# Optimization experiments

Measured on AMD Instinct MI355X. Metric: run time of the kernel, lower is better.

The kernel has to match this reference:

```python
import jax, jax.numpy as jnp
import numpy as np

N_NODES = 50000
IN_C, HID_C, OUT_C = 128, 128, 64
N_EDGES = 800000
N_LABEL = 200000
BN_EPS = 1e-5


def setup_inputs() -> dict:
    key = jax.random.key(0)
    ks = jax.random.split(key, 12)
    s = lambda fan_in: 1.0 / np.sqrt(fan_in)
    return {
        "x": jax.random.normal(ks[0], (N_NODES, IN_C), dtype=jnp.float32),
        "edge_index": jax.random.randint(ks[1], (2, N_EDGES), 0, N_NODES, dtype=jnp.int64),
        "edge_label_index": jax.random.randint(ks[2], (2, N_LABEL), 0, N_NODES, dtype=jnp.int64),
        # SAGEConv1: lin_l (neighbor branch, with bias) and lin_r (root branch, no bias)
        "W1l": jax.random.uniform(ks[3], (IN_C, HID_C), jnp.float32, -s(IN_C), s(IN_C)),
        "W1r": jax.random.uniform(ks[4], (IN_C, HID_C), jnp.float32, -s(IN_C), s(IN_C)),
        "b1": jax.random.uniform(ks[5], (HID_C,), jnp.float32, -s(IN_C), s(IN_C)),
        # BatchNorm1d(hidden)
        "gamma": jnp.ones((HID_C,), jnp.float32),
        "beta": jnp.zeros((HID_C,), jnp.float32),
        # SAGEConv2
        "W2l": jax.random.uniform(ks[6], (HID_C, OUT_C), jnp.float32, -s(HID_C), s(HID_C)),
        "W2r": jax.random.uniform(ks[7], (HID_C, OUT_C), jnp.float32, -s(HID_C), s(HID_C)),
        "b2": jax.random.uniform(ks[8], (OUT_C,), jnp.float32, -s(HID_C), s(HID_C)),
    }


def _sage_conv(x, edge_index, Wl, Wr, b):
    # PyG SAGEConv(aggr='mean'): out = lin_l(mean_{j->i} x_j) + lin_r(x_i)
    src, dst = edge_index[0], edge_index[1]
    n = x.shape[0]
    agg = jax.ops.segment_sum(x[src], dst, num_segments=n)          # [N, C]
    cnt = jax.ops.segment_sum(jnp.ones((src.shape[0],), x.dtype), dst, num_segments=n)
    mean = agg / jnp.maximum(cnt, 1.0)[:, None]                     # isolated nodes -> 0
    return mean @ Wl + x @ Wr + b


def _batchnorm(h, gamma, beta):
    mu = jnp.mean(h, axis=0)
    var = jnp.mean((h - mu) ** 2, axis=0)  # biased variance (torch BN training math)
    return gamma * (h - mu) * jax.lax.rsqrt(var + BN_EPS) + beta


def reference(x, edge_index, edge_label_index, W1l, W1r, b1, gamma, beta, W2l, W2r, b2):
    h = _sage_conv(x, edge_index, W1l, W1r, b1)
    h = jax.nn.relu(_batchnorm(h, gamma, beta))
    # dropout is identity in inference mode
    z = _sage_conv(h, edge_index, W2l, W2r, b2)
    src = z[edge_label_index[0]]
    dst = z[edge_label_index[1]]
    return jnp.sum(src * dst, axis=-1)  # [E_label]
```

## Files before the change

kernel.cpp:

```cpp
#include <hip/hip_runtime.h>

constexpr int N_NODES = 50000;
constexpr int IN_C    = 128;
constexpr int HID_C   = 128;
constexpr int OUT_C   = 64;
constexpr int N_EDGES = 800000;
constexpr int N_LABEL = 200000;
constexpr float BN_EPS = 1e-5f;
constexpr int NCHUNK  = (N_NODES + 256) / 256 + 1;
constexpr int BN_BLOCKS = 512;
constexpr int BN_RPH    = 13;

typedef __attribute__((ext_vector_type(8))) short bf16x8;
typedef __attribute__((ext_vector_type(4))) float f32x4;

__device__ __forceinline__ float bf_lo(unsigned v) {
    union { unsigned u; float f; } t; t.u = v << 16; return t.f;
}
__device__ __forceinline__ float bf_hi(unsigned v) {
    union { unsigned u; float f; } t; t.u = v & 0xffff0000u; return t.f;
}
__device__ __forceinline__ float bf1(unsigned short u) {
    union { unsigned u; float f; } t; t.u = ((unsigned)u) << 16; return t.f;
}
__device__ __forceinline__ unsigned short f2bf(float f) {
    union { float f; unsigned u; } t; t.f = f;
    unsigned r = t.u + 0x7fffu + ((t.u >> 16) & 1u);
    return (unsigned short)(r >> 16);
}

__global__ void hist_kernel(const int* __restrict__ dst, int* __restrict__ deg,
                            int* __restrict__ rank) {
    int e = blockIdx.x * blockDim.x + threadIdx.x;
    if (e < N_EDGES) rank[e] = atomicAdd(&deg[dst[e]], 1);
}

__global__ void chunk_sum_kernel(const int* __restrict__ deg, int* __restrict__ bsum) {
    int i = blockIdx.x * 256 + threadIdx.x;
    int v = deg[i];
    #pragma unroll
    for (int o = 32; o > 0; o >>= 1) v += __shfl_down(v, o, 64);
    __shared__ int ws[4];
    if ((threadIdx.x & 63) == 0) ws[threadIdx.x >> 6] = v;
    __syncthreads();
    if (threadIdx.x == 0) bsum[blockIdx.x] = ws[0] + ws[1] + ws[2] + ws[3];
}

__global__ void scan_bsum_kernel(const int* __restrict__ bsum, int* __restrict__ boff) {
    __shared__ int t[256];
    int tid = threadIdx.x;
    t[tid] = (tid < NCHUNK) ? bsum[tid] : 0;
    __syncthreads();
    for (int o = 1; o < 256; o <<= 1) {
        int v = t[tid];
        int add = (tid >= o) ? t[tid - o] : 0;
        __syncthreads();
        t[tid] = v + add;
        __syncthreads();
    }
    boff[tid] = (tid == 0) ? 0 : t[tid - 1];
}

__global__ void scan_final_kernel(const int* __restrict__ deg, const int* __restrict__ boff,
                                  int* __restrict__ off) {
    __shared__ int t[256];
    int tid = threadIdx.x;
    int i = blockIdx.x * 256 + tid;
    int d = deg[i];
    t[tid] = d;
    __syncthreads();
    for (int o = 1; o < 256; o <<= 1) {
        int v = t[tid];
        int add = (tid >= o) ? t[tid - o] : 0;
        __syncthreads();
        t[tid] = v + add;
        __syncthreads();
    }
    int excl = boff[blockIdx.x] + t[tid] - d;
    if (i <= N_NODES) off[i] = excl;
}

__global__ void scatter_kernel(const int* __restrict__ src, const int* __restrict__ dst,
                               const int* __restrict__ off, const int* __restrict__ rank,
                               int* __restrict__ csr_src) {
    int e = blockIdx.x * blockDim.x + threadIdx.x;
    if (e < N_EDGES) csr_src[off[dst[e]] + rank[e]] = src[e];
}

__global__ void prep_B(const float* __restrict__ Wl, const float* __restrict__ Wr,
                       short* __restrict__ Bp, int C) {
    int f = blockIdx.x * 256 + threadIdx.x;
    if (f >= 128 * C) return;
    int HALF = C >> 1;
    int j = f & 7;
    int l = (f >> 3) & 63;
    int ktnt = f >> 9;
    int kt = ktnt & 3, nt = ktnt >> 2;
    int n = nt * 16 + (l & 15);
    int k = kt * 32 + ((l >> 4) << 3) + j;
    float v = (n < HALF) ? Wl[k * HALF + n] : Wr[k * HALF + (n - HALF)];
    Bp[f] = (short)f2bf(v);
}

template <int MODE>
__global__ __launch_bounds__(256) void mfma_gemm(
    const float* __restrict__ A, const short* __restrict__ Bp,
    const float* __restrict__ bias, const float* __restrict__ ss,
    unsigned short* __restrict__ outL,
    float* __restrict__ outHf, unsigned short* __restrict__ outHb)
{
    constexpr int C    = (MODE == 0) ? 256 : 128;
    constexpr int NT   = C / 16;
    constexpr int HALF = C / 2;
    constexpr int CHUNKS = 128 * C / 8;

    __shared__ short sB[128 * C];

    {
        const float4* bp4 = reinterpret_cast<const float4*>(Bp);
        float4* sb4 = reinterpret_cast<float4*>(sB);
        #pragma unroll
        for (int i = 0; i < CHUNKS / 256; ++i)
            sb4[i * 256 + threadIdx.x] = bp4[i * 256 + threadIdx.x];
    }

    int tid  = threadIdx.x;
    int wid  = tid >> 6, lane = tid & 63;
    int m0   = blockIdx.x * 64 + wid * 16;
    int row  = m0 + (lane & 15);
    int rowc = (row < N_NODES) ? row : (N_NODES - 1);
    const float* ap = A + (long long)rowc * 128;
    int kbase = (lane >> 4) * 8;

    bf16x8 a[4];
    #pragma unroll
    for (int kt = 0; kt < 4; ++kt) {
        int k0 = kt * 32 + kbase;
        float4 u0 = *reinterpret_cast<const float4*>(ap + k0);
        float4 u1 = *reinterpret_cast<const float4*>(ap + k0 + 4);
        float v[8] = {u0.x, u0.y, u0.z, u0.w, u1.x, u1.y, u1.z, u1.w};
        if (MODE == 1) {
            float4 s0 = *reinterpret_cast<const float4*>(ss + k0);
            float4 s1 = *reinterpret_cast<const float4*>(ss + k0 + 4);
            float4 t0 = *reinterpret_cast<const float4*>(ss + 128 + k0);
            float4 t1 = *reinterpret_cast<const float4*>(ss + 128 + k0 + 4);
            float sc[8] = {s0.x, s0.y, s0.z, s0.w, s1.x, s1.y, s1.z, s1.w};
            float sh[8] = {t0.x, t0.y, t0.z, t0.w, t1.x, t1.y, t1.z, t1.w};
            #pragma unroll
            for (int j = 0; j < 8; ++j) v[j] = fmaxf(v[j] * sc[j] + sh[j], 0.f);
        }
        #pragma unroll
        for (int j = 0; j < 8; ++j) a[kt][j] = (short)f2bf(v[j]);
    }

    __syncthreads();

    f32x4 acc[NT] = {};
    #pragma unroll
    for (int kt = 0; kt < 4; ++kt) {
        #pragma unroll
        for (int nt = 0; nt < NT; ++nt) {
            bf16x8 b = *reinterpret_cast<const bf16x8*>(
                sB + ((((nt << 2) + kt) * 64 + lane) << 3));
            acc[nt] = __builtin_amdgcn_mfma_f32_16x16x32_bf16(a[kt], b, acc[nt], 0, 0, 0);
        }
    }

    int r0 = m0 + ((lane >> 4) << 2);
    int nl = lane & 15;
    #pragma unroll
    for (int nt = 0; nt < NT; ++nt) {
        int col = nt * 16 + nl;
        float bb = (col >= HALF) ? bias[col - HALF] : 0.f;
        #pragma unroll
        for (int j = 0; j < 4; ++j) {
            int r = r0 + j;
            if (r >= N_NODES) continue;
            float vv = acc[nt][j];
            if (MODE == 0) {
                if (col < HALF) outL[(long long)r * 128 + col] = f2bf(vv);
                else            outHf[(long long)r * 128 + (col - HALF)] = vv + bb;
            } else {
                if (col < HALF) outL[(long long)r * 64 + col] = f2bf(vv);
                else            outHb[(long long)r * 64 + (col - HALF)] = f2bf(vv + bb);
            }
        }
    }
}

__global__ __launch_bounds__(256) void agg_mean_add_128(
    const int* __restrict__ off, const int* __restrict__ csr_src,
    const uint2* __restrict__ y2, float* __restrict__ h) {
    int node = blockIdx.x * 4 + (threadIdx.x >> 6);
    if (node >= N_NODES) return;
    int lane = threadIdx.x & 63;
    int half = lane >> 5;
    int c8   = lane & 31;
    int beg = off[node], end = off[node + 1];
    float s0 = 0.f, s1 = 0.f, s2 = 0.f, s3 = 0.f;
    int i = beg + half;
    for (; i + 6 < end; i += 8) {
        uint2 v0 = y2[(long long)csr_src[i]     * 32 + c8];
        uint2 v1 = y2[(long long)csr_src[i + 2] * 32 + c8];
        uint2 v2 = y2[(long long)csr_src[i + 4] * 32 + c8];
        uint2 v3 = y2[(long long)csr_src[i + 6] * 32 + c8];
        s0 += bf_lo(v0.x) + bf_lo(v1.x) + bf_lo(v2.x) + bf_lo(v3.x);
        s1 += bf_hi(v0.x) + bf_hi(v1.x) + bf_hi(v2.x) + bf_hi(v3.x);
        s2 += bf_lo(v0.y) + bf_lo(v1.y) + bf_lo(v2.y) + bf_lo(v3.y);
        s3 += bf_hi(v0.y) + bf_hi(v1.y) + bf_hi(v2.y) + bf_hi(v3.y);
    }
    for (; i < end; i += 2) {
        uint2 v0 = y2[(long long)csr_src[i] * 32 + c8];
        s0 += bf_lo(v0.x); s1 += bf_hi(v0.x);
        s2 += bf_lo(v0.y); s3 += bf_hi(v0.y);
    }
    s0 += __shfl_down(s0, 32);
    s1 += __shfl_down(s1, 32);
    s2 += __shfl_down(s2, 32);
    s3 += __shfl_down(s3, 32);
    if (half == 0) {
        float inv = (end > beg) ? 1.0f / (float)(end - beg) : 0.f;
        float4* hp = reinterpret_cast<float4*>(h + (long long)node * 128 + c8 * 4);
        float4 hv = *hp;
        hv.x += s0 * inv; hv.y += s1 * inv; hv.z += s2 * inv; hv.w += s3 * inv;
        *hp = hv;
    }
}

__global__ __launch_bounds__(256) void bn_stats_partial(
    const float* __restrict__ h, float* __restrict__ partial) {
    int tid = threadIdx.x;
    int wid = tid >> 6;
    int lane = tid & 63;
    int half = lane >> 5;
    int c4   = lane & 31;
    int hw   = (blockIdx.x << 3) + (wid << 1) + half;
    int r0   = hw * BN_RPH;

    float4 v[BN_RPH];
    #pragma unroll
    for (int j = 0; j < BN_RPH; ++j) {
        int r = r0 + j;
        if (r < N_NODES)
            v[j] = *reinterpret_cast<const float4*>(h + (long long)r * 128 + c4 * 4);
        else
            v[j] = float4{0.f, 0.f, 0.f, 0.f};
    }
    float s[4] = {0.f, 0.f, 0.f, 0.f}, q[4] = {0.f, 0.f, 0.f, 0.f};
    #pragma unroll
    for (int j = 0; j < BN_RPH; ++j) {
        s[0] += v[j].x; q[0] += v[j].x * v[j].x;
        s[1] += v[j].y; q[1] += v[j].y * v[j].y;
        s[2] += v[j].z; q[2] += v[j].z * v[j].z;
        s[3] += v[j].w; q[3] += v[j].w * v[j].w;
    }
    #pragma unroll
    for (int j = 0; j < 4; ++j) {
        s[j] += __shfl_down(s[j], 32);
        q[j] += __shfl_down(q[j], 32);
    }
    __shared__ float ls[4][32][8];
    if (half == 0) {
        #pragma unroll
        for (int j = 0; j < 4; ++j) { ls[wid][c4][j] = s[j]; ls[wid][c4][4 + j] = q[j]; }
    }
    __syncthreads();
    if (tid < 32) {
        #pragma unroll
        for (int j = 0; j < 8; ++j) {
            float a = ls[0][tid][j] + ls[1][tid][j] + ls[2][tid][j] + ls[3][tid][j];
            partial[blockIdx.x * 256 + (j < 4 ? 0 : 128) + tid * 4 + (j & 3)] = a;
        }
    }
}

__global__ void bn_stats_reduce(const float* __restrict__ partial,
                                float* __restrict__ sums) {
    int t = threadIdx.x;
    int b0 = blockIdx.x * (BN_BLOCKS / 16);
    float a = 0.f;
    #pragma unroll 8
    for (int b = b0; b < b0 + BN_BLOCKS / 16; ++b)
        a += partial[b * 256 + t];
    atomicAdd(&sums[t], a);
}

__global__ void bn_finalize_kernel(const float* __restrict__ sums,
                                   const float* __restrict__ gamma,
                                   const float* __restrict__ beta,
                                   float* __restrict__ ss) {
    int c = threadIdx.x;
    float mu  = sums[c] * (1.0f / N_NODES);
    float var = sums[128 + c] * (1.0f / N_NODES) - mu * mu;
    float sc = gamma[c] * rsqrtf(var + BN_EPS);
    ss[c] = sc;
    ss[128 + c] = beta[c] - mu * sc;
}

__global__ __launch_bounds__(256) void agg_mean_add_64(
    const int* __restrict__ off, const int* __restrict__ csr_src,
    const uint2* __restrict__ t2l2, const uint2* __restrict__ t2r2,
    uint2* __restrict__ z2) {
    int node = blockIdx.x * 4 + (threadIdx.x >> 6);
    if (node >= N_NODES) return;
    int lane = threadIdx.x & 63;
    int grp  = lane >> 4;
    int c8   = lane & 15;
    int beg = off[node], end = off[node + 1];
    float s0 = 0.f, s1 = 0.f, s2 = 0.f, s3 = 0.f;
    int i = beg + grp;
    for (; i + 4 < end; i += 8) {
        uint2 v0 = t2l2[(long long)csr_src[i]     * 16 + c8];
        uint2 v1 = t2l2[(long long)csr_src[i + 4] * 16 + c8];
        s0 += bf_lo(v0.x) + bf_lo(v1.x);
        s1 += bf_hi(v0.x) + bf_hi(v1.x);
        s2 += bf_lo(v0.y) + bf_lo(v1.y);
        s3 += bf_hi(v0.y) + bf_hi(v1.y);
    }
    for (; i < end; i += 4) {
        uint2 v0 = t2l2[(long long)csr_src[i] * 16 + c8];
        s0 += bf_lo(v0.x); s1 += bf_hi(v0.x);
        s2 += bf_lo(v0.y); s3 += bf_hi(v0.y);
    }
    s0 += __shfl_down(s0, 16); s1 += __shfl_down(s1, 16);
    s2 += __shfl_down(s2, 16); s3 += __shfl_down(s3, 16);
    s0 += __shfl_down(s0, 32); s1 += __shfl_down(s1, 32);
    s2 += __shfl_down(s2, 32); s3 += __shfl_down(s3, 32);
    if (grp == 0) {
        float inv = (end > beg) ? 1.0f / (float)(end - beg) : 0.f;
        uint2 rv = t2r2[(long long)node * 16 + c8];
        float r0 = bf_lo(rv.x) + s0 * inv;
        float r1 = bf_hi(rv.x) + s1 * inv;
        float r2 = bf_lo(rv.y) + s2 * inv;
        float r3 = bf_hi(rv.y) + s3 * inv;
        uint2 o;
        o.x = (unsigned)f2bf(r0) | ((unsigned)f2bf(r1) << 16);
        o.y = (unsigned)f2bf(r2) | ((unsigned)f2bf(r3) << 16);
        z2[(long long)node * 16 + c8] = o;
    }
}

__global__ void edge_dot_kernel(const int* __restrict__ eli,
                                const unsigned short* __restrict__ z,
                                float* __restrict__ out) {
    long long gid = (long long)blockIdx.x * blockDim.x + threadIdx.x;
    int l = (int)(gid >> 4);
    int lane = (int)(gid & 15);
    if (l >= N_LABEL) return;
    int s = eli[l];
    int d = eli[N_LABEL + l];
    uint2 av = *reinterpret_cast<const uint2*>(z + (long long)s * 64 + lane * 4);
    uint2 bv = *reinterpret_cast<const uint2*>(z + (long long)d * 64 + lane * 4);
    float p = bf_lo(av.x) * bf_lo(bv.x) + bf_hi(av.x) * bf_hi(bv.x)
            + bf_lo(av.y) * bf_lo(bv.y) + bf_hi(av.y) * bf_hi(bv.y);
    p += __shfl_down(p, 8, 16);
    p += __shfl_down(p, 4, 16);
    p += __shfl_down(p, 2, 16);
    p += __shfl_down(p, 1, 16);
    if (lane == 0) out[l] = p;
}

extern "C" void kernel_launch(void* const* d_in, const int* in_sizes, int n_in,
                              void* d_out, int out_size, void* d_ws, size_t ws_size,
                              hipStream_t stream) {
    const float* x     = (const float*)d_in[0];
    const int*   ei    = (const int*)d_in[1];
    const int*   eli   = (const int*)d_in[2];
    const float* W1l   = (const float*)d_in[3];
    const float* W1r   = (const float*)d_in[4];
    const float* b1    = (const float*)d_in[5];
    const float* gamma = (const float*)d_in[6];
    const float* beta  = (const float*)d_in[7];
    const float* W2l   = (const float*)d_in[8];
    const float* W2r   = (const float*)d_in[9];
    const float* b2    = (const float*)d_in[10];
    float* out = (float*)d_out;

    const int* src  = ei;
    const int* dstv = ei + N_EDGES;

    int* ideg  = (int*)d_ws;
    int* ioff  = ideg + 50432;
    int* ibsum = ioff + 50056;
    int* iboff = ibsum + 256;
    int* icsr  = iboff + 256;
    unsigned short* y1  = (unsigned short*)(icsr + 800000);
    float*          h   = (float*)(y1 + 6400000);
    unsigned short* t2l = (unsigned short*)(h + 6400000);
    unsigned short* t2r = t2l + 3200000;
    unsigned short* z   = t2r + 3200000;
    float* sums = (float*)(z + 3200000);
    float* ss   = sums + 256;
    short* Bp1  = (short*)(ss + 256);
    short* Bp2  = Bp1 + 32768;
    float* bnpart = (float*)(Bp2 + 16384);
    int* irank = (int*)y1;

    hipMemsetAsync(ideg, 0, 50432 * sizeof(int), stream);
    hipMemsetAsync(sums, 0, 256 * sizeof(float), stream);

    prep_B<<<(128 * 256 + 255) / 256, 256, 0, stream>>>(W1l, W1r, Bp1, 256);
    prep_B<<<(128 * 128 + 255) / 256, 256, 0, stream>>>(W2l, W2r, Bp2, 128);

    hist_kernel<<<(N_EDGES + 255) / 256, 256, 0, stream>>>(dstv, ideg, irank);
    chunk_sum_kernel<<<NCHUNK, 256, 0, stream>>>(ideg, ibsum);
    scan_bsum_kernel<<<1, 256, 0, stream>>>(ibsum, iboff);
    scan_final_kernel<<<NCHUNK, 256, 0, stream>>>(ideg, iboff, ioff);
    scatter_kernel<<<(N_EDGES + 255) / 256, 256, 0, stream>>>(src, dstv, ioff, irank, icsr);

    const int GEMM_GRID = (N_NODES + 63) / 64;

    mfma_gemm<0><<<GEMM_GRID, 256, 0, stream>>>(x, Bp1, b1, ss, y1, h, nullptr);
    agg_mean_add_128<<<(N_NODES + 3) / 4, 256, 0, stream>>>(
        ioff, icsr, (const uint2*)y1, h);

    bn_stats_partial<<<BN_BLOCKS, 256, 0, stream>>>(h, bnpart);
    bn_stats_reduce<<<16, 256, 0, stream>>>(bnpart, sums);
    bn_finalize_kernel<<<1, 128, 0, stream>>>(sums, gamma, beta, ss);

    mfma_gemm<1><<<GEMM_GRID, 256, 0, stream>>>(h, Bp2, b2, ss, t2l, nullptr, t2r);
    agg_mean_add_64<<<(N_NODES + 3) / 4, 256, 0, stream>>>(
        ioff, icsr, (const uint2*)t2l, (const uint2*)t2r, (uint2*)z);

    edge_dot_kernel<<<((long long)N_LABEL * 16 + 255) / 256, 256, 0, stream>>>(eli, z, out);
}
```

Baseline: 200.7 us.

## Store layer-1 neighbor projection in fp8 and hidden activations in bf16

The layer-1 neighbor-branch GEMM output is now stored as a custom 8-bit float (scaled e4m3-like encoding) instead of bf16, which halves the bytes gathered per edge in the first aggregation. The root-branch hidden tensor h becomes bf16 instead of fp32, so the aggregation read-modify-write, the BN stats pass and the second GEMM's A load all move half the data. The aggregation loop is restructured so four 16-lane groups each read 8 channels per edge. The cost is reduced numerical precision in the intermediate activations, which may push error toward tolerance limits.

```diff
diff --git a/kernel.cpp b/kernel.cpp
--- a/kernel.cpp
+++ b/kernel.cpp
@@ -20,13 +20,25 @@
 __device__ __forceinline__ float bf_hi(unsigned v) {
     union { unsigned u; float f; } t; t.u = v & 0xffff0000u; return t.f;
 }
-__device__ __forceinline__ float bf1(unsigned short u) {
-    union { unsigned u; float f; } t; t.u = ((unsigned)u) << 16; return t.f;
-}
 __device__ __forceinline__ unsigned short f2bf(float f) {
     union { float f; unsigned u; } t; t.f = f;
     unsigned r = t.u + 0x7fffu + ((t.u >> 16) & 1u);
     return (unsigned short)(r >> 16);
+}
+__device__ __forceinline__ unsigned pack2bf(float a, float b) {
+    return (unsigned)f2bf(a) | ((unsigned)f2bf(b) << 16);
+}
+
+__device__ __forceinline__ float fp8_f32(unsigned b) {
+    union { unsigned u; float f; } t;
+    t.u = ((b & 0x80u) << 24) | ((b & 0x7Fu) << 20);
+    return t.f * 0x1p120f;
+}
+__device__ __forceinline__ unsigned f32_fp8(float x) {
+    union { float f; unsigned u; } t; t.f = x * 0x1p-120f;
+    unsigned au = t.u & 0x7FFFFFFFu;
+    unsigned r = au + 0x7FFFFu + ((au >> 20) & 1u);
+    return ((r >> 20) & 0x7Fu) | ((t.u >> 24) & 0x80u);
 }
 
 __global__ void hist_kernel(const int* __restrict__ dst, int* __restrict__ deg,
@@ -104,10 +116,11 @@
 
 template <int MODE>
 __global__ __launch_bounds__(256) void mfma_gemm(
-    const float* __restrict__ A, const short* __restrict__ Bp,
+    const void* __restrict__ Ain, const short* __restrict__ Bp,
     const float* __restrict__ bias, const float* __restrict__ ss,
-    unsigned short* __restrict__ outL,
-    float* __restrict__ outHf, unsigned short* __restrict__ outHb)
+    unsigned char* __restrict__ outFp8,
+    unsigned short* __restrict__ outL16,
+    unsigned short* __restrict__ outH16)
 {
     constexpr int C    = (MODE == 0) ? 256 : 128;
     constexpr int NT   = C / 16;
@@ -129,17 +142,24 @@
     int m0   = blockIdx.x * 64 + wid * 16;
     int row  = m0 + (lane & 15);
     int rowc = (row < N_NODES) ? row : (N_NODES - 1);
-    const float* ap = A + (long long)rowc * 128;
     int kbase = (lane >> 4) * 8;
 
     bf16x8 a[4];
     #pragma unroll
     for (int kt = 0; kt < 4; ++kt) {
         int k0 = kt * 32 + kbase;
-        float4 u0 = *reinterpret_cast<const float4*>(ap + k0);
-        float4 u1 = *reinterpret_cast<const float4*>(ap + k0 + 4);
-        float v[8] = {u0.x, u0.y, u0.z, u0.w, u1.x, u1.y, u1.z, u1.w};
-        if (MODE == 1) {
+        float v[8];
+        if (MODE == 0) {
+            const float* ap = (const float*)Ain + (long long)rowc * 128;
+            float4 u0 = *reinterpret_cast<const float4*>(ap + k0);
+            float4 u1 = *reinterpret_cast<const float4*>(ap + k0 + 4);
+            v[0]=u0.x; v[1]=u0.y; v[2]=u0.z; v[3]=u0.w;
+            v[4]=u1.x; v[5]=u1.y; v[6]=u1.z; v[7]=u1.w;
+        } else {
+            const unsigned short* ap = (const unsigned short*)Ain + (long long)rowc * 128;
+            uint4 w = *reinterpret_cast<const uint4*>(ap + k0);
+            v[0]=bf_lo(w.x); v[1]=bf_hi(w.x); v[2]=bf_lo(w.y); v[3]=bf_hi(w.y);
+            v[4]=bf_lo(w.z); v[5]=bf_hi(w.z); v[6]=bf_lo(w.w); v[7]=bf_hi(w.w);
             float4 s0 = *reinterpret_cast<const float4*>(ss + k0);
             float4 s1 = *reinterpret_cast<const float4*>(ss + k0 + 4);
             float4 t0 = *reinterpret_cast<const float4*>(ss + 128 + k0);
@@ -178,11 +198,11 @@
             if (r >= N_NODES) continue;
             float vv = acc[nt][j];
             if (MODE == 0) {
-                if (col < HALF) outL[(long long)r * 128 + col] = f2bf(vv);
-                else            outHf[(long long)r * 128 + (col - HALF)] = vv + bb;
+                if (col < HALF) outFp8[(long long)r * 128 + col] = (unsigned char)f32_fp8(vv);
+                else            outH16[(long long)r * 128 + (col - HALF)] = f2bf(vv + bb);
             } else {
-                if (col < HALF) outL[(long long)r * 64 + col] = f2bf(vv);
-                else            outHb[(long long)r * 64 + (col - HALF)] = f2bf(vv + bb);
+                if (col < HALF) outL16[(long long)r * 64 + col] = f2bf(vv);
+                else            outH16[(long long)r * 64 + (col - HALF)] = f2bf(vv + bb);
             }
         }
     }
@@ -190,45 +210,50 @@
 
 __global__ __launch_bounds__(256) void agg_mean_add_128(
     const int* __restrict__ off, const int* __restrict__ csr_src,
-    const uint2* __restrict__ y2, float* __restrict__ h) {
+    const uint2* __restrict__ y8, uint4* __restrict__ h4) {
     int node = blockIdx.x * 4 + (threadIdx.x >> 6);
     if (node >= N_NODES) return;
     int lane = threadIdx.x & 63;
-    int half = lane >> 5;
-    int c8   = lane & 31;
+    int grp  = lane >> 4;
+    int c8   = lane & 15;
     int beg = off[node], end = off[node + 1];
-    float s0 = 0.f, s1 = 0.f, s2 = 0.f, s3 = 0.f;
-    int i = beg + half;
-    for (; i + 6 < end; i += 8) {
-        uint2 v0 = y2[(long long)csr_src[i]     * 32 + c8];
-        uint2 v1 = y2[(long long)csr_src[i + 2] * 32 + c8];
-        uint2 v2 = y2[(long long)csr_src[i + 4] * 32 + c8];
-        uint2 v3 = y2[(long long)csr_src[i + 6] * 32 + c8];
-        s0 += bf_lo(v0.x) + bf_lo(v1.x) + bf_lo(v2.x) + bf_lo(v3.x);
-        s1 += bf_hi(v0.x) + bf_hi(v1.x) + bf_hi(v2.x) + bf_hi(v3.x);
-        s2 += bf_lo(v0.y) + bf_lo(v1.y) + bf_lo(v2.y) + bf_lo(v3.y);
-        s3 += bf_hi(v0.y) + bf_hi(v1.y) + bf_hi(v2.y) + bf_hi(v3.y);
-    }
-    for (; i < end; i += 2) {
-        uint2 v0 = y2[(long long)csr_src[i] * 32 + c8];
-        s0 += bf_lo(v0.x); s1 += bf_hi(v0.x);
-        s2 += bf_lo(v0.y); s3 += bf_hi(v0.y);
-    }
-    s0 += __shfl_down(s0, 32);
-    s1 += __shfl_down(s1, 32);
-    s2 += __shfl_down(s2, 32);
-    s3 += __shfl_down(s3, 32);
-    if (half == 0) {
+    float s[8] = {0.f, 0.f, 0.f, 0.f, 0.f, 0.f, 0.f, 0.f};
+    int i = beg + grp;
+    for (; i + 4 < end; i += 8) {
+        uint2 v0 = y8[(long long)csr_src[i]     * 16 + c8];
+        uint2 v1 = y8[(long long)csr_src[i + 4] * 16 + c8];
+        #pragma unroll
+        for (int j = 0; j < 4; ++j) {
+            s[j]     += fp8_f32((v0.x >> (8 * j)) & 0xFFu) + fp8_f32((v1.x >> (8 * j)) & 0xFFu);
+            s[4 + j] += fp8_f32((v0.y >> (8 * j)) & 0xFFu) + fp8_f32((v1.y >> (8 * j)) & 0xFFu);
+        }
+    }
+    for (; i < end; i += 4) {
+        uint2 v0 = y8[(long long)csr_src[i] * 16 + c8];
+        #pragma unroll
+        for (int j = 0; j < 4; ++j) {
+            s[j]     += fp8_f32((v0.x >> (8 * j)) & 0xFFu);
+            s[4 + j] += fp8_f32((v0.y >> (8 * j)) & 0xFFu);
+        }
+    }
+    #pragma unroll
+    for (int j = 0; j < 8; ++j) {
+        s[j] += __shfl_down(s[j], 16);
+        s[j] += __shfl_down(s[j], 32);
+    }
+    if (grp == 0) {
         float inv = (end > beg) ? 1.0f / (float)(end - beg) : 0.f;
-        float4* hp = reinterpret_cast<float4*>(h + (long long)node * 128 + c8 * 4);
-        float4 hv = *hp;
-        hv.x += s0 * inv; hv.y += s1 * inv; hv.z += s2 * inv; hv.w += s3 * inv;
-        *hp = hv;
+        uint4 hv = h4[(long long)node * 16 + c8];
+        hv.x = pack2bf(bf_lo(hv.x) + s[0] * inv, bf_hi(hv.x) + s[1] * inv);
+        hv.y = pack2bf(bf_lo(hv.y) + s[2] * inv, bf_hi(hv.y) + s[3] * inv);
+        hv.z = pack2bf(bf_lo(hv.z) + s[4] * inv, bf_hi(hv.z) + s[5] * inv);
+        hv.w = pack2bf(bf_lo(hv.w) + s[6] * inv, bf_hi(hv.w) + s[7] * inv);
+        h4[(long long)node * 16 + c8] = hv;
     }
 }
 
 __global__ __launch_bounds__(256) void bn_stats_partial(
-    const float* __restrict__ h, float* __restrict__ partial) {
+    const uint2* __restrict__ h2, float* __restrict__ partial) {
     int tid = threadIdx.x;
     int wid = tid >> 6;
     int lane = tid & 63;
@@ -237,22 +262,21 @@
     int hw   = (blockIdx.x << 3) + (wid << 1) + half;
     int r0   = hw * BN_RPH;
 
-    float4 v[BN_RPH];
+    uint2 v[BN_RPH];
     #pragma unroll
     for (int j = 0; j < BN_RPH; ++j) {
         int r = r0 + j;
-        if (r < N_NODES)
-            v[j] = *reinterpret_cast<const float4*>(h + (long long)r * 128 + c4 * 4);
-        else
-            v[j] = float4{0.f, 0.f, 0.f, 0.f};
+        v[j] = (r < N_NODES) ? h2[(long long)r * 32 + c4] : uint2{0u, 0u};
     }
     float s[4] = {0.f, 0.f, 0.f, 0.f}, q[4] = {0.f, 0.f, 0.f, 0.f};
     #pragma unroll
     for (int j = 0; j < BN_RPH; ++j) {
-        s[0] += v[j].x; q[0] += v[j].x * v[j].x;
-        s[1] += v[j].y; q[1] += v[j].y * v[j].y;
-        s[2] += v[j].z; q[2] += v[j].z * v[j].z;
-        s[3] += v[j].w; q[3] += v[j].w * v[j].w;
+        float a0 = bf_lo(v[j].x), a1 = bf_hi(v[j].x);
+        float a2 = bf_lo(v[j].y), a3 = bf_hi(v[j].y);
+        s[0] += a0; q[0] += a0 * a0;
+        s[1] += a1; q[1] += a1 * a1;
+        s[2] += a2; q[2] += a2 * a2;
+        s[3] += a3; q[3] += a3 * a3;
     }
     #pragma unroll
     for (int j = 0; j < 4; ++j) {
@@ -329,13 +353,9 @@
     if (grp == 0) {
         float inv = (end > beg) ? 1.0f / (float)(end - beg) : 0.f;
         uint2 rv = t2r2[(long long)node * 16 + c8];
-        float r0 = bf_lo(rv.x) + s0 * inv;
-        float r1 = bf_hi(rv.x) + s1 * inv;
-        float r2 = bf_lo(rv.y) + s2 * inv;
-        float r3 = bf_hi(rv.y) + s3 * inv;
         uint2 o;
-        o.x = (unsigned)f2bf(r0) | ((unsigned)f2bf(r1) << 16);
-        o.y = (unsigned)f2bf(r2) | ((unsigned)f2bf(r3) << 16);
+        o.x = pack2bf(bf_lo(rv.x) + s0 * inv, bf_hi(rv.x) + s1 * inv);
+        o.y = pack2bf(bf_lo(rv.y) + s2 * inv, bf_hi(rv.y) + s3 * inv);
         z2[(long long)node * 16 + c8] = o;
     }
 }
@@ -384,9 +404,9 @@
     int* ibsum = ioff + 50056;
     int* iboff = ibsum + 256;
     int* icsr  = iboff + 256;
-    unsigned short* y1  = (unsigned short*)(icsr + 800000);
-    float*          h   = (float*)(y1 + 6400000);
-    unsigned short* t2l = (unsigned short*)(h + 6400000);
+    unsigned char*  y1  = (unsigned char*)(icsr + 800000);
+    unsigned short* h   = (unsigned short*)(y1 + 6400000);
+    unsigned short* t2l = h + 6400000;
     unsigned short* t2r = t2l + 3200000;
     unsigned short* z   = t2r + 3200000;
     float* sums = (float*)(z + 3200000);
@@ -410,15 +430,15 @@
 
     const int GEMM_GRID = (N_NODES + 63) / 64;
 
-    mfma_gemm<0><<<GEMM_GRID, 256, 0, stream>>>(x, Bp1, b1, ss, y1, h, nullptr);
+    mfma_gemm<0><<<GEMM_GRID, 256, 0, stream>>>(x, Bp1, b1, ss, y1, nullptr, h);
     agg_mean_add_128<<<(N_NODES + 3) / 4, 256, 0, stream>>>(
-        ioff, icsr, (const uint2*)y1, h);
-
-    bn_stats_partial<<<BN_BLOCKS, 256, 0, stream>>>(h, bnpart);
+        ioff, icsr, (const uint2*)y1, (uint4*)h);
+
+    bn_stats_partial<<<BN_BLOCKS, 256, 0, stream>>>((const uint2*)h, bnpart);
     bn_stats_reduce<<<16, 256, 0, stream>>>(bnpart, sums);
     bn_finalize_kernel<<<1, 128, 0, stream>>>(sums, gamma, beta, ss);
 
-    mfma_gemm<1><<<GEMM_GRID, 256, 0, stream>>>(h, Bp2, b2, ss, t2l, nullptr, t2r);
+    mfma_gemm<1><<<GEMM_GRID, 256, 0, stream>>>(h, Bp2, b2, ss, nullptr, t2l, t2r);
     agg_mean_add_64<<<(N_NODES + 3) / 4, 256, 0, stream>>>(
         ioff, icsr, (const uint2*)t2l, (const uint2*)t2r, (uint2*)z);
 
```

New measurement: 190.4 us. -5.2%, faster.
